# Performance work log

Measured on AMD Instinct MI355X. Metric: run time of the kernel, lower is better.

Reference implementation:

```python
import jax, jax.numpy as jnp
import numpy as np

D_K = 64


def setup_inputs() -> dict:
    key = jax.random.key(0)
    k1, k2, k3 = jax.random.split(key, 3)
    B, H, S, DK, DV = 2, 16, 2048, 64, 64
    Q = jax.random.normal(k1, (B, H, S, DK), dtype=jnp.float32)
    K = jax.random.normal(k2, (B, H, S, DK), dtype=jnp.float32)
    V = jax.random.normal(k3, (B, H, S, DV), dtype=jnp.float32)
    # causal mask, True = keep (broadcasts over batch/head as in the torch code)
    mask = jnp.tril(jnp.ones((S, S), dtype=bool))
    return {"Q": Q, "K": K, "V": V, "mask": mask}


def reference(Q, K, V, mask):
    # scores[b,h,c,v] = sum_k Q[b,h,c,k] * K[b,h,v,k]
    scores = jnp.einsum('bhck,bhvk->bhcv', Q, K)
    # torch: B = inf at ~mask; scores - B  ->  -inf at masked positions
    scores = jnp.where(mask, scores, -jnp.inf)
    # scale applied AFTER masking, exactly as in the torch forward
    probs = jax.nn.softmax(scores / jnp.sqrt(jnp.float32(D_K)), axis=-1)
    return probs @ V
```

## Files before the change

### kernel.cpp

```cpp
#include <hip/hip_runtime.h>
#include <hip/hip_bf16.h>

#define S_LEN 2048
#define DIM   64
#define NBH   32
#define NQT   32
#define NQB   16
#define TILE_SH 12288
#define WS_NEED ((size_t)NBH * NQT * TILE_SH * sizeof(short))

typedef __attribute__((ext_vector_type(4))) float f32x4;
typedef __attribute__((ext_vector_type(8))) short s16x8;
typedef __attribute__((ext_vector_type(4))) short s16x4;

#define MFMA_B16(A,B,C) __builtin_amdgcn_mfma_f32_16x16x32_bf16(A,B,C,0,0,0)
#define EX2(x) __builtin_amdgcn_exp2f(x)

__device__ __forceinline__ short f2bf(float x){
  union{float f;unsigned u;} v; v.f=x;
  unsigned r = v.u + 0x7FFFu + ((v.u>>16)&1u);
  return (short)(r>>16);
}
__device__ __forceinline__ float bf2f(short s){
  union{float f;unsigned u;} v; v.u=((unsigned)(unsigned short)s)<<16;
  return v.f;
}
__device__ __forceinline__ unsigned packbf(float a, float b){
  __hip_bfloat162 h = __float22bfloat162_rn(make_float2(a, b));
  union { __hip_bfloat162 h; unsigned u; } cv; cv.h = h; return cv.u;
}
__device__ __forceinline__ int swz(int row){
  return (((row&7) ^ ((row>>2)&7)) << 3);
}

__global__ __launch_bounds__(256) void prep_kv(
    const float* __restrict__ K, const float* __restrict__ V, short* __restrict__ W)
{
  __shared__ short Vl[4096];
  const int b  = blockIdx.x;
  const int bh = b >> 5, t = b & 31;
  const float* Kt = K + ((size_t)bh * S_LEN + t * 64) * DIM;
  const float* Vt = V + ((size_t)bh * S_LEN + t * 64) * DIM;
  short* Wt = W + (size_t)b * TILE_SH;
  const int tid = threadIdx.x;

#pragma unroll
  for (int i = 0; i < 2; ++i) {
    const int m = i * 256 + tid;
    const int r = m >> 3, g = m & 7;
    const int c0 = (g << 3) ^ swz(r);
    float x[8];
    *(f32x4*)&x[0] = *(const f32x4*)(Kt + r * DIM + c0);
    *(f32x4*)&x[4] = *(const f32x4*)(Kt + r * DIM + c0 + 4);
    s16x8 hi, lo;
#pragma unroll
    for (int j = 0; j < 8; ++j) {
      short h = f2bf(x[j]);
      hi[j] = h;
      lo[j] = f2bf(x[j] - bf2f(h));
    }
    *(s16x8*)&Wt[m * 8]        = hi;
    *(s16x8*)&Wt[4096 + m * 8] = lo;
  }

  {
    const int r2 = (tid >> 3) << 1;
    const int cb = (tid & 7) << 3;
    float x0[8], x1[8];
    *(f32x4*)&x0[0] = *(const f32x4*)(Vt + r2 * DIM + cb);
    *(f32x4*)&x0[4] = *(const f32x4*)(Vt + r2 * DIM + cb + 4);
    *(f32x4*)&x1[0] = *(const f32x4*)(Vt + (r2 + 1) * DIM + cb);
    *(f32x4*)&x1[4] = *(const f32x4*)(Vt + (r2 + 1) * DIM + cb + 4);
#pragma unroll
    for (int j = 0; j < 8; ++j) {
      const int c = cb + j;
      const int y = r2 ^ swz(c);
      ((unsigned*)Vl)[(c * 64 + y) >> 1] = packbf(x0[j], x1[j]);
    }
  }
  __syncthreads();
#pragma unroll
  for (int i = 0; i < 2; ++i) {
    const int p = (i * 256 + tid) * 8;
    *(s16x8*)&Wt[8192 + p] = *(const s16x8*)&Vl[p];
  }
}

__device__ __forceinline__ void stage24(const short* __restrict__ src, short* dst,
                                        int w, int l) {
#pragma unroll
  for (int q = 0; q < 3; ++q) {
    const int off = (q * 8 + w) << 10;
    __builtin_amdgcn_global_load_lds(
        (const __attribute__((address_space(1))) unsigned*)((const char*)src + off + l * 16),
        (__attribute__((address_space(3))) unsigned*)((char*)dst + off),
        16, 0, 0);
  }
}

__device__ __forceinline__ void qk_tile(f32x4 acc[4], const short* __restrict__ bK,
                                        const s16x8 qh[2], const s16x8 ql[2],
                                        int l15, int lg)
{
  const short* bKl = bK + 4096;
#pragma unroll
  for (int f = 0; f < 4; ++f) acc[f] = f32x4{0.f,0.f,0.f,0.f};
#pragma unroll
  for (int f = 0; f < 4; ++f) {
    const int kr = f * 16 + l15;
#pragma unroll
    for (int s = 0; s < 2; ++s) {
      const int dk = (((lg << 3) + (s << 5)) ^ swz(kr));
      s16x8 ah = *(const s16x8*)&bK [kr * DIM + dk];
      s16x8 al = *(const s16x8*)&bKl[kr * DIM + dk];
      acc[f] = MFMA_B16(ah, qh[s], acc[f]);
      acc[f] = MFMA_B16(ah, ql[s], acc[f]);
      acc[f] = MFMA_B16(al, qh[s], acc[f]);
    }
  }
}

__device__ __forceinline__ void sm_update(f32x4 acc[4], f32x4 o[4], float& m, float& lsum,
                                          int kv0, int qg, int lg, float SC)
{
  const bool anymask = (kv0 + 63 > qg);
  float pm = -INFINITY;
#pragma unroll
  for (int f = 0; f < 4; ++f)
#pragma unroll
    for (int r = 0; r < 4; ++r) {
      float zz = acc[f][r] * SC;
      if (anymask && (kv0 + f * 16 + (lg << 2) + r) > qg) zz = -INFINITY;
      acc[f][r] = zz;
      pm = fmaxf(pm, zz);
    }
  pm = fmaxf(pm, __shfl_xor(pm, 16));
  pm = fmaxf(pm, __shfl_xor(pm, 32));
  if (!__all(pm <= m)) {
    const float mn = fmaxf(m, pm);
    const float al = EX2(m - mn);
    m = mn; lsum *= al;
#pragma unroll
    for (int d = 0; d < 4; ++d) o[d] *= al;
  }
  float rs = 0.f;
#pragma unroll
  for (int f = 0; f < 4; ++f)
#pragma unroll
    for (int r = 0; r < 4; ++r) {
      const float pv = EX2(acc[f][r] - m);
      acc[f][r] = pv;
      rs += pv;
    }
  rs += __shfl_xor(rs, 16);
  rs += __shfl_xor(rs, 32);
  lsum += rs;
}

__device__ __forceinline__ void pv_tile(const f32x4 p[4], f32x4 o[4],
                                        const short* __restrict__ bVt,
                                        int l15, int lg, int src0, int src1, bool hiH)
{
  unsigned U[4][2];
#pragma unroll
  for (int f = 0; f < 4; ++f) {
    U[f][0] = packbf(p[f][0], p[f][1]);
    U[f][1] = packbf(p[f][2], p[f][3]);
  }
#pragma unroll
  for (int s = 0; s < 2; ++s) {
    unsigned a0 = __shfl(U[2*s][0], src0), a1 = __shfl(U[2*s+1][0], src0);
    unsigned b0 = __shfl(U[2*s][1], src0), b1 = __shfl(U[2*s+1][1], src0);
    unsigned c0 = __shfl(U[2*s][0], src1), c1 = __shfl(U[2*s+1][0], src1);
    unsigned d0 = __shfl(U[2*s][1], src1), d1 = __shfl(U[2*s+1][1], src1);
    union { unsigned u[4]; s16x8 v; } pb;
    pb.u[0] = hiH ? a1 : a0;
    pb.u[1] = hiH ? b1 : b0;
    pb.u[2] = hiH ? c1 : c0;
    pb.u[3] = hiH ? d1 : d0;
    const int kv8 = (lg << 3) + (s << 5);
#pragma unroll
    for (int d = 0; d < 4; ++d) {
      const int dv = d * 16 + l15;
      s16x8 vf = *(const s16x8*)&bVt[dv * DIM + (kv8 ^ swz(dv))];
      o[d] = MFMA_B16(vf, pb.v, o[d]);
    }
  }
}

__global__ __launch_bounds__(512, 4) void fattn_main(
    const float* __restrict__ Qg, float* __restrict__ Og, const short* __restrict__ W)
{
  __shared__ __attribute__((aligned(16))) short buf[3][TILE_SH];

  const int bid = blockIdx.x;
  const int bh = bid & 31;
  const int idx = bid >> 5;
  const int qt = (idx < 8) ? (15 - idx) : (idx - 8);

  const int tid = threadIdx.x;
  const int w = tid >> 6, l = tid & 63;
  const int l15 = l & 15, lg = l >> 4;

  const short* Wb = W + (size_t)bh * NQT * TILE_SH;
  const float* Qb = Qg + (size_t)bh * S_LEN * DIM;
  float*       Ob = Og + (size_t)bh * S_LEN * DIM;

  const int qg = qt * 128 + w * 16 + l15;
  const float SC = 0.125f * 1.44269504088896f;

  s16x8 qh[2], ql[2];
#pragma unroll
  for (int s = 0; s < 2; ++s) {
    const float* qp = Qb + (size_t)qg * DIM + (lg << 3) + s * 32;
    float qv[8];
    *(f32x4*)&qv[0] = *(const f32x4*)qp;
    *(f32x4*)&qv[4] = *(const f32x4*)(qp + 4);
#pragma unroll
    for (int j = 0; j < 8; ++j) {
      short h = f2bf(qv[j]);
      qh[s][j] = h;
      ql[s][j] = f2bf(qv[j] - bf2f(h));
    }
  }

  f32x4 o[4];
#pragma unroll
  for (int d = 0; d < 4; ++d) o[d] = f32x4{0.f,0.f,0.f,0.f};
  float m = -INFINITY, lsum = 0.f;

  const int src0 = l15 + ((lg & 1) << 5);
  const int src1 = src0 + 16;
  const bool hiH = (lg >= 2);

  const int nt = 2 * qt + 2;

  short* b0 = buf[0];
  short* b1 = buf[1];
  short* b2 = buf[2];
  stage24(Wb, b0, w, l);
  __syncthreads();
  stage24(Wb + TILE_SH, b1, w, l);
  f32x4 acc[4];
  qk_tile(acc, b0, qh, ql, l15, lg);
  __syncthreads();

  for (int t = 0; t < nt - 1; ++t) {
    if (t + 2 < nt) stage24(Wb + (size_t)(t + 2) * TILE_SH, b2, w, l);
    sm_update(acc, o, m, lsum, t * 64, qg, lg, SC);
    f32x4 acc2[4];
    qk_tile(acc2, b1, qh, ql, l15, lg);
    pv_tile(acc, o, b0 + 8192, l15, lg, src0, src1, hiH);
#pragma unroll
    for (int f = 0; f < 4; ++f) acc[f] = acc2[f];
    short* tmp = b0; b0 = b1; b1 = b2; b2 = tmp;
    __syncthreads();
  }
  sm_update(acc, o, m, lsum, (nt - 1) * 64, qg, lg, SC);
  pv_tile(acc, o, b0 + 8192, l15, lg, src0, src1, hiH);

  const float inv = 1.0f / lsum;
#pragma unroll
  for (int d = 0; d < 4; ++d) {
    f32x4 ov;
#pragma unroll
    for (int r = 0; r < 4; ++r) ov[r] = o[d][r] * inv;
    *(f32x4*)(Ob + (size_t)qg * DIM + d * 16 + (lg << 2)) = ov;
  }
}

#define QBLK  64
#define KVBLK 64
#define NPAIR (NQT/2)
#define NBLK  (NBH*NPAIR)

__global__ __launch_bounds__(256) void fattn_fb(
    const float* __restrict__ Qg, const float* __restrict__ Kg,
    const float* __restrict__ Vg, float* __restrict__ Og)
{
  __shared__ __attribute__((aligned(16))) short Khi[KVBLK*DIM];
  __shared__ __attribute__((aligned(16))) short Klo[KVBLK*DIM];
  __shared__ __attribute__((aligned(16))) short Vt [DIM*KVBLK];
  __shared__ __attribute__((aligned(16))) short Pl [4*16*KVBLK];

  int bid0 = blockIdx.x;
  int bid  = (bid0 & 7) * (NBLK/8) + (bid0 >> 3);
  int bh   = bid / NPAIR;
  int pr   = bid % NPAIR;
  const int tid = threadIdx.x;
  const int w = tid >> 6, l = tid & 63, l15 = l & 15, lg = l >> 4;
  const float* Qb = Qg + (size_t)bh * S_LEN * DIM;
  const float* Kb = Kg + (size_t)bh * S_LEN * DIM;
  const float* Vb = Vg + (size_t)bh * S_LEN * DIM;
  float*       Ob = Og + (size_t)bh * S_LEN * DIM;
  const float SC = 0.125f * 1.44269504088896f;

  for (int half = 0; half < 2; ++half) {
    const int qt = half ? (NQT - 1 - pr) : pr;
    const int qg = qt * QBLK + w * 16 + l15;
    s16x8 qh[2], ql[2];
#pragma unroll
    for (int s = 0; s < 2; ++s) {
      const float* qp = Qb + (size_t)qg * DIM + (lg << 3) + s * 32;
      float qv[8];
      *(f32x4*)&qv[0] = *(const f32x4*)qp;
      *(f32x4*)&qv[4] = *(const f32x4*)(qp + 4);
#pragma unroll
      for (int j = 0; j < 8; ++j) {
        short h = f2bf(qv[j]); qh[s][j] = h; ql[s][j] = f2bf(qv[j] - bf2f(h));
      }
    }
    f32x4 o[4];
#pragma unroll
    for (int d = 0; d < 4; ++d) o[d] = f32x4{0.f,0.f,0.f,0.f};
    float m = -INFINITY, lsum = 0.f;
    const int ntiles = qt + 1;
    for (int t = 0; t < ntiles; ++t) {
      const int kv0 = t * KVBLK;
      __syncthreads();
      {
        const int row = tid >> 4, c4 = (tid & 15) << 2;
#pragma unroll
        for (int i = 0; i < 4; ++i) {
          const int r = row + (i << 4);
          const f32x4 kv4 = *(const f32x4*)(Kb + (size_t)(kv0 + r) * DIM + c4);
          const f32x4 vv4 = *(const f32x4*)(Vb + (size_t)(kv0 + r) * DIM + c4);
          const int cs = c4 ^ swz(r);
          s16x4 kh, kl;
#pragma unroll
          for (int j = 0; j < 4; ++j) { short h = f2bf(kv4[j]); kh[j] = h; kl[j] = f2bf(kv4[j] - bf2f(h)); }
          *(s16x4*)&Khi[r * DIM + cs] = kh;
          *(s16x4*)&Klo[r * DIM + cs] = kl;
#pragma unroll
          for (int j = 0; j < 4; ++j) { const int dv = c4 + j; Vt[dv * KVBLK + (r ^ swz(dv))] = f2bf(vv4[j]); }
        }
      }
      __syncthreads();
      f32x4 acc[4];
#pragma unroll
      for (int f = 0; f < 4; ++f) acc[f] = f32x4{0.f,0.f,0.f,0.f};
#pragma unroll
      for (int f = 0; f < 4; ++f) {
        const int kr = f * 16 + l15;
#pragma unroll
        for (int s = 0; s < 2; ++s) {
          const int dk = (((lg << 3) + (s << 5)) ^ swz(kr));
          s16x8 ah = *(const s16x8*)&Khi[kr * DIM + dk];
          s16x8 al = *(const s16x8*)&Klo[kr * DIM + dk];
          acc[f] = MFMA_B16(ah, qh[s], acc[f]);
          acc[f] = MFMA_B16(ah, ql[s], acc[f]);
          acc[f] = MFMA_B16(al, qh[s], acc[f]);
        }
      }
      const bool diag = (t == qt);
      float z[4][4];
#pragma unroll
      for (int f = 0; f < 4; ++f)
#pragma unroll
        for (int r = 0; r < 4; ++r) {
          float zz = acc[f][r] * SC;
          if (diag && (kv0 + f * 16 + (lg << 2) + r) > qg) zz = -INFINITY;
          z[f][r] = zz;
        }
      float pm = z[0][0];
#pragma unroll
      for (int f = 0; f < 4; ++f)
#pragma unroll
        for (int r = 0; r < 4; ++r) pm = fmaxf(pm, z[f][r]);
      pm = fmaxf(pm, __shfl_xor(pm, 16));
      pm = fmaxf(pm, __shfl_xor(pm, 32));
      const float mn = fmaxf(m, pm);
      const float alpha = EX2(m - mn);
      float p[4][4]; float rs = 0.f;
#pragma unroll
      for (int f = 0; f < 4; ++f)
#pragma unroll
        for (int r = 0; r < 4; ++r) { const float pv = EX2(z[f][r] - mn); p[f][r] = pv; rs += pv; }
      rs += __shfl_xor(rs, 16);
      rs += __shfl_xor(rs, 32);
      lsum = lsum * alpha + rs;
      m = mn;
#pragma unroll
      for (int d = 0; d < 4; ++d) o[d] *= alpha;
      short* Pw = &Pl[w * 16 * KVBLK];
#pragma unroll
      for (int f = 0; f < 4; ++f) {
        s16x4 pk;
#pragma unroll
        for (int r = 0; r < 4; ++r) pk[r] = f2bf(p[f][r]);
        const int kvc = (f * 16 + (lg << 2)) ^ swz(l15);
        *(s16x4*)&Pw[l15 * KVBLK + kvc] = pk;
      }
#pragma unroll
      for (int s = 0; s < 2; ++s) {
        const int kv8 = (lg << 3) + s * 32;
        s16x8 pf = *(const s16x8*)&Pw[l15 * KVBLK + (kv8 ^ swz(l15))];
#pragma unroll
        for (int d = 0; d < 4; ++d) {
          const int dv = d * 16 + l15;
          s16x8 vf = *(const s16x8*)&Vt[dv * KVBLK + (kv8 ^ swz(dv))];
          o[d] = MFMA_B16(vf, pf, o[d]);
        }
      }
    }
    const float inv = 1.0f / lsum;
#pragma unroll
    for (int d = 0; d < 4; ++d) {
      f32x4 ov;
#pragma unroll
      for (int r = 0; r < 4; ++r) ov[r] = o[d][r] * inv;
      *(f32x4*)(Ob + (size_t)qg * DIM + d * 16 + (lg << 2)) = ov;
    }
  }
}

extern "C" void kernel_launch(void* const* d_in, const int* in_sizes, int n_in,
                              void* d_out, int out_size, void* d_ws, size_t ws_size,
                              hipStream_t stream) {
  const float* Q = (const float*)d_in[0];
  const float* K = (const float*)d_in[1];
  const float* V = (const float*)d_in[2];
  float* O = (float*)d_out;
  if (ws_size >= WS_NEED) {
    short* W = (short*)d_ws;
    prep_kv  <<<dim3(NBH * NQT), dim3(256), 0, stream>>>(K, V, W);
    fattn_main<<<dim3(NBH * NQB), dim3(512), 0, stream>>>(Q, O, W);
  } else {
    fattn_fb<<<dim3(NBLK), dim3(256), 0, stream>>>(Q, K, V, O);
  }
}
```

Baseline: 163.8 us.

## Split causal attention KV range into chunks with separate merge kernel

Adds a split-KV (flash-decoding style) path. Each 128-row query tile is divided into KV chunks of at most eight tiles, giving 40 balanced chunks per head, each computed by its own block. Partial outputs and (max, sum) pairs go to the workspace and a merge kernel combines them, which targets the load imbalance and long tail of causal tiles. The cost is an extra launch plus round-trip traffic for the partials, and the path only runs if the workspace is large enough. prep_kv is also reworked to use 512 threads with one element per thread.

Result: slower. 175.3 us (+7.0%).

```diff
diff --git a/kernel.cpp b/kernel.cpp
--- a/kernel.cpp
+++ b/kernel.cpp
@@ -7,7 +7,12 @@
 #define NQT   32
 #define NQB   16
 #define TILE_SH 12288
-#define WS_NEED ((size_t)NBH * NQT * TILE_SH * sizeof(short))
+#define IMG_B  ((size_t)NBH * NQT * TILE_SH * sizeof(short))
+#define NCH    40
+#define OPART_B ((size_t)NBH * NCH * 128 * 64 * sizeof(float))
+#define ML_B    ((size_t)NBH * NCH * 128 * 2 * sizeof(float))
+#define WS_NEED  IMG_B
+#define WS2_NEED (IMG_B + OPART_B + ML_B)
 
 typedef __attribute__((ext_vector_type(4))) float f32x4;
 typedef __attribute__((ext_vector_type(8))) short s16x8;
@@ -15,6 +20,24 @@
 
 #define MFMA_B16(A,B,C) __builtin_amdgcn_mfma_f32_16x16x32_bf16(A,B,C,0,0,0)
 #define EX2(x) __builtin_amdgcn_exp2f(x)
+
+__device__ static const int CH_QT[NCH] = {
+  15,15,15,15, 14,14,14, 13,13,13, 12,12,12, 11,11,11, 10,10, 9,9, 8,8, 7,7,
+  6, 5, 4, 3,
+  14,10,6,2,
+  13,9,5,1,
+  12,8,4,0 };
+__device__ static const int CH_C0[NCH] = {
+  0,8,16,24, 0,8,16, 0,8,16, 0,8,16, 0,8,16, 0,8, 0,8, 0,8, 0,8,
+  0, 0, 0, 0,
+  24,16,8,0,
+  24,16,8,0,
+  24,16,8,0 };
+__device__ static const int MG[16][4] = {
+  {39,-1,-1,-1},{35,-1,-1,-1},{31,-1,-1,-1},{27,-1,-1,-1},
+  {26,38,-1,-1},{25,34,-1,-1},{24,30,-1,-1},{22,23,-1,-1},
+  {20,21,37,-1},{18,19,33,-1},{16,17,29,-1},{13,14,15,-1},
+  {10,11,12,36},{7,8,9,32},{4,5,6,28},{0,1,2,3} };
 
 __device__ __forceinline__ short f2bf(float x){
   union{float f;unsigned u;} v; v.f=x;
@@ -33,7 +56,7 @@
   return (((row&7) ^ ((row>>2)&7)) << 3);
 }
 
-__global__ __launch_bounds__(256) void prep_kv(
+__global__ __launch_bounds__(512) void prep_kv(
     const float* __restrict__ K, const float* __restrict__ V, short* __restrict__ W)
 {
   __shared__ short Vl[4096];
@@ -44,10 +67,8 @@
   short* Wt = W + (size_t)b * TILE_SH;
   const int tid = threadIdx.x;
 
-#pragma unroll
-  for (int i = 0; i < 2; ++i) {
-    const int m = i * 256 + tid;
-    const int r = m >> 3, g = m & 7;
+  {
+    const int r = tid >> 3, g = tid & 7;
     const int c0 = (g << 3) ^ swz(r);
     float x[8];
     *(f32x4*)&x[0] = *(const f32x4*)(Kt + r * DIM + c0);
@@ -59,31 +80,23 @@
       hi[j] = h;
       lo[j] = f2bf(x[j] - bf2f(h));
     }
-    *(s16x8*)&Wt[m * 8]        = hi;
-    *(s16x8*)&Wt[4096 + m * 8] = lo;
-  }
-
+    *(s16x8*)&Wt[tid * 8]        = hi;
+    *(s16x8*)&Wt[4096 + tid * 8] = lo;
+  }
   {
-    const int r2 = (tid >> 3) << 1;
+    const int r = tid >> 3;
     const int cb = (tid & 7) << 3;
-    float x0[8], x1[8];
-    *(f32x4*)&x0[0] = *(const f32x4*)(Vt + r2 * DIM + cb);
-    *(f32x4*)&x0[4] = *(const f32x4*)(Vt + r2 * DIM + cb + 4);
-    *(f32x4*)&x1[0] = *(const f32x4*)(Vt + (r2 + 1) * DIM + cb);
-    *(f32x4*)&x1[4] = *(const f32x4*)(Vt + (r2 + 1) * DIM + cb + 4);
+    float x[8];
+    *(f32x4*)&x[0] = *(const f32x4*)(Vt + r * DIM + cb);
+    *(f32x4*)&x[4] = *(const f32x4*)(Vt + r * DIM + cb + 4);
 #pragma unroll
     for (int j = 0; j < 8; ++j) {
       const int c = cb + j;
-      const int y = r2 ^ swz(c);
-      ((unsigned*)Vl)[(c * 64 + y) >> 1] = packbf(x0[j], x1[j]);
+      Vl[c * 64 + (r ^ swz(c))] = f2bf(x[j]);
     }
   }
   __syncthreads();
-#pragma unroll
-  for (int i = 0; i < 2; ++i) {
-    const int p = (i * 256 + tid) * 8;
-    *(s16x8*)&Wt[8192 + p] = *(const s16x8*)&Vl[p];
-  }
+  *(s16x8*)&Wt[8192 + tid * 8] = *(const s16x8*)&Vl[tid * 8];
 }
 
 __device__ __forceinline__ void stage24(const short* __restrict__ src, short* dst,
@@ -188,25 +201,29 @@
   }
 }
 
-__global__ __launch_bounds__(512, 4) void fattn_main(
-    const float* __restrict__ Qg, float* __restrict__ Og, const short* __restrict__ W)
+__global__ __launch_bounds__(512, 4) void fattn_chunk(
+    const float* __restrict__ Qg, const short* __restrict__ W,
+    float* __restrict__ Opart, float* __restrict__ ML)
 {
   __shared__ __attribute__((aligned(16))) short buf[3][TILE_SH];
 
   const int bid = blockIdx.x;
+  const int i  = bid >> 5;
   const int bh = bid & 31;
-  const int idx = bid >> 5;
-  const int qt = (idx < 8) ? (15 - idx) : (idx - 8);
+  const int qt = CH_QT[i];
+  const int c0 = CH_C0[i];
+  const int t1 = min(2 * qt + 2, c0 + 8);
+  const int len = t1 - c0;
 
   const int tid = threadIdx.x;
   const int w = tid >> 6, l = tid & 63;
   const int l15 = l & 15, lg = l >> 4;
 
-  const short* Wb = W + (size_t)bh * NQT * TILE_SH;
+  const short* Wb = W + ((size_t)bh * NQT + c0) * TILE_SH;
   const float* Qb = Qg + (size_t)bh * S_LEN * DIM;
-  float*       Ob = Og + (size_t)bh * S_LEN * DIM;
-
-  const int qg = qt * 128 + w * 16 + l15;
+
+  const int row = w * 16 + l15;
+  const int qg = qt * 128 + row;
   const float SC = 0.125f * 1.44269504088896f;
 
   s16x8 qh[2], ql[2];
@@ -232,8 +249,6 @@
   const int src0 = l15 + ((lg & 1) << 5);
   const int src1 = src0 + 16;
   const bool hiH = (lg >= 2);
-
-  const int nt = 2 * qt + 2;
 
   short* b0 = buf[0];
   short* b1 = buf[1];
@@ -245,6 +260,119 @@
   qk_tile(acc, b0, qh, ql, l15, lg);
   __syncthreads();
 
+  for (int t = 0; t < len - 1; ++t) {
+    if (t + 2 < len) stage24(Wb + (size_t)(t + 2) * TILE_SH, b2, w, l);
+    sm_update(acc, o, m, lsum, (c0 + t) * 64, qg, lg, SC);
+    f32x4 acc2[4];
+    qk_tile(acc2, b1, qh, ql, l15, lg);
+    pv_tile(acc, o, b0 + 8192, l15, lg, src0, src1, hiH);
+#pragma unroll
+    for (int f = 0; f < 4; ++f) acc[f] = acc2[f];
+    short* tmp = b0; b0 = b1; b1 = b2; b2 = tmp;
+    __syncthreads();
+  }
+  sm_update(acc, o, m, lsum, (t1 - 1) * 64, qg, lg, SC);
+  pv_tile(acc, o, b0 + 8192, l15, lg, src0, src1, hiH);
+
+  float* op = Opart + ((size_t)(bh * NCH + i) * 128 + row) * 64;
+#pragma unroll
+  for (int d = 0; d < 4; ++d)
+    *(f32x4*)(op + d * 16 + (lg << 2)) = o[d];
+  if (lg == 0) {
+    float2 ml2 = make_float2(m, lsum);
+    *(float2*)&ML[((size_t)(bh * NCH + i) * 128 + row) * 2] = ml2;
+  }
+}
+
+__global__ __launch_bounds__(256) void fattn_merge(
+    const float* __restrict__ Opart, const float* __restrict__ ML,
+    float* __restrict__ Og)
+{
+  const int bid = blockIdx.x;
+  const int qt = bid >> 5, bh = bid & 31;
+  const int tid = threadIdx.x;
+  const int dv4 = (tid & 15) << 2;
+  const int r0  = tid >> 4;
+
+#pragma unroll 1
+  for (int pass = 0; pass < 8; ++pass) {
+    const int row = pass * 16 + r0;
+    float mv[4], lv[4];
+    float M = -INFINITY;
+#pragma unroll
+    for (int k = 0; k < 4; ++k) { mv[k] = -INFINITY; lv[k] = 0.f; }
+#pragma unroll
+    for (int k = 0; k < 4; ++k) {
+      const int s = MG[qt][k];
+      if (s >= 0) {
+        const float2 ml2 = *(const float2*)&ML[((size_t)(bh * NCH + s) * 128 + row) * 2];
+        mv[k] = ml2.x; lv[k] = ml2.y;
+        M = fmaxf(M, ml2.x);
+      }
+    }
+    float L = 0.f;
+    f32x4 acc = f32x4{0.f,0.f,0.f,0.f};
+#pragma unroll
+    for (int k = 0; k < 4; ++k) {
+      const int s = MG[qt][k];
+      if (s >= 0) {
+        const float wgt = EX2(mv[k] - M);
+        L += lv[k] * wgt;
+        const f32x4 ov = *(const f32x4*)&Opart[((size_t)(bh * NCH + s) * 128 + row) * 64 + dv4];
+        acc += ov * wgt;
+      }
+    }
+    const float inv = 1.0f / L;
+    f32x4 outv;
+#pragma unroll
+    for (int r = 0; r < 4; ++r) outv[r] = acc[r] * inv;
+    *(f32x4*)(Og + ((size_t)bh * S_LEN + qt * 128 + row) * DIM + dv4) = outv;
+  }
+}
+
+__global__ __launch_bounds__(512, 4) void fattn_main(
+    const float* __restrict__ Qg, float* __restrict__ Og, const short* __restrict__ W)
+{
+  __shared__ __attribute__((aligned(16))) short buf[3][TILE_SH];
+  const int bid = blockIdx.x;
+  const int bh = bid & 31;
+  const int idx = bid >> 5;
+  const int qt = (idx < 8) ? (15 - idx) : (idx - 8);
+  const int tid = threadIdx.x;
+  const int w = tid >> 6, l = tid & 63;
+  const int l15 = l & 15, lg = l >> 4;
+  const short* Wb = W + (size_t)bh * NQT * TILE_SH;
+  const float* Qb = Qg + (size_t)bh * S_LEN * DIM;
+  float*       Ob = Og + (size_t)bh * S_LEN * DIM;
+  const int qg = qt * 128 + w * 16 + l15;
+  const float SC = 0.125f * 1.44269504088896f;
+  s16x8 qh[2], ql[2];
+#pragma unroll
+  for (int s = 0; s < 2; ++s) {
+    const float* qp = Qb + (size_t)qg * DIM + (lg << 3) + s * 32;
+    float qv[8];
+    *(f32x4*)&qv[0] = *(const f32x4*)qp;
+    *(f32x4*)&qv[4] = *(const f32x4*)(qp + 4);
+#pragma unroll
+    for (int j = 0; j < 8; ++j) {
+      short h = f2bf(qv[j]); qh[s][j] = h; ql[s][j] = f2bf(qv[j] - bf2f(h));
+    }
+  }
+  f32x4 o[4];
+#pragma unroll
+  for (int d = 0; d < 4; ++d) o[d] = f32x4{0.f,0.f,0.f,0.f};
+  float m = -INFINITY, lsum = 0.f;
+  const int src0 = l15 + ((lg & 1) << 5);
+  const int src1 = src0 + 16;
+  const bool hiH = (lg >= 2);
+  const int nt = 2 * qt + 2;
+  short* b0 = buf[0]; short* b1 = buf[1]; short* b2 = buf[2];
+  stage24(Wb, b0, w, l);
+  __syncthreads();
+  stage24(Wb + TILE_SH, b1, w, l);
+  f32x4 acc[4];
+  qk_tile(acc, b0, qh, ql, l15, lg);
+  __syncthreads();
   for (int t = 0; t < nt - 1; ++t) {
     if (t + 2 < nt) stage24(Wb + (size_t)(t + 2) * TILE_SH, b2, w, l);
     sm_update(acc, o, m, lsum, t * 64, qg, lg, SC);
@@ -258,7 +386,6 @@
   }
   sm_update(acc, o, m, lsum, (nt - 1) * 64, qg, lg, SC);
   pv_tile(acc, o, b0 + 8192, l15, lg, src0, src1, hiH);
-
   const float inv = 1.0f / lsum;
 #pragma unroll
   for (int d = 0; d < 4; ++d) {
@@ -282,7 +409,6 @@
   __shared__ __attribute__((aligned(16))) short Klo[KVBLK*DIM];
   __shared__ __attribute__((aligned(16))) short Vt [DIM*KVBLK];
   __shared__ __attribute__((aligned(16))) short Pl [4*16*KVBLK];
-
   int bid0 = blockIdx.x;
   int bid  = (bid0 & 7) * (NBLK/8) + (bid0 >> 3);
   int bh   = bid / NPAIR;
@@ -294,7 +420,6 @@
   const float* Vb = Vg + (size_t)bh * S_LEN * DIM;
   float*       Ob = Og + (size_t)bh * S_LEN * DIM;
   const float SC = 0.125f * 1.44269504088896f;
-
   for (int half = 0; half < 2; ++half) {
     const int qt = half ? (NQT - 1 - pr) : pr;
     const int qg = qt * QBLK + w * 16 + l15;
@@ -421,9 +546,16 @@
   const float* K = (const float*)d_in[1];
   const float* V = (const float*)d_in[2];
   float* O = (float*)d_out;
-  if (ws_size >= WS_NEED) {
+  if (ws_size >= WS2_NEED) {
+    short* W      = (short*)d_ws;
+    float* Opart  = (float*)((char*)d_ws + IMG_B);
+    float* ML     = Opart + (size_t)NBH * NCH * 128 * 64;
+    prep_kv    <<<dim3(NBH * NQT), dim3(512), 0, stream>>>(K, V, W);
+    fattn_chunk<<<dim3(NBH * NCH), dim3(512), 0, stream>>>(Q, W, Opart, ML);
+    fattn_merge<<<dim3(NBH * NQB), dim3(256), 0, stream>>>(Opart, ML, O);
+  } else if (ws_size >= WS_NEED) {
     short* W = (short*)d_ws;
-    prep_kv  <<<dim3(NBH * NQT), dim3(256), 0, stream>>>(K, V, W);
+    prep_kv  <<<dim3(NBH * NQT), dim3(512), 0, stream>>>(K, V, W);
     fattn_main<<<dim3(NBH * NQB), dim3(512), 0, stream>>>(Q, O, W);
   } else {
     fattn_fb<<<dim3(NBLK), dim3(256), 0, stream>>>(Q, K, V, O);
```
